# Kernel tuning notes

Measured on AMD Instinct MI355X. Metric: run time of the kernel, lower is better.

Reference implementation:

```python
import jax, jax.numpy as jnp
import numpy as np

BN_EPS = 1e-5

def _bn_relu(x, gamma, beta):
    # BatchNorm1d in training mode: batch stats over (B, N) per channel
    mean = jnp.mean(x, axis=(0, 1), keepdims=True)
    var = jnp.var(x, axis=(0, 1), keepdims=True)
    return jax.nn.relu((x - mean) * jax.lax.rsqrt(var + BN_EPS) * gamma + beta)

def setup_inputs() -> dict:
    key = jax.random.key(0)
    ks = jax.random.split(key, 8)
    B, N, S, C1, C2 = 8, 8192, 2048, 128, 256
    return {
        'xyz1': jax.random.normal(ks[0], (B, N, 3), jnp.float32),
        'xyz2': jax.random.normal(ks[1], (B, S, 3), jnp.float32),
        'points1': jax.random.normal(ks[2], (B, N, C1), jnp.float32),
        'points2': jax.random.normal(ks[3], (B, S, C2), jnp.float32),
        'w0': jax.random.normal(ks[4], (256, C1 + C2), jnp.float32) * 0.02,
        'b0': jnp.zeros((256,), jnp.float32),
        'g0': jnp.ones((256,), jnp.float32),
        'be0': jnp.zeros((256,), jnp.float32),
        'w1': jax.random.normal(ks[5], (128, 256), jnp.float32) * 0.02,
        'b1': jnp.zeros((128,), jnp.float32),
        'g1': jnp.ones((128,), jnp.float32),
        'be1': jnp.zeros((128,), jnp.float32),
    }

def reference(xyz1, xyz2, points1, points2, w0, b0, g0, be0, w1, b1, g1, be1):
    # squared pairwise distances [B, N, S]
    sq = (jnp.sum(xyz1 * xyz1, -1)[:, :, None]
          - 2.0 * jnp.einsum('bnc,bmc->bnm', xyz1, xyz2)
          + jnp.sum(xyz2 * xyz2, -1)[:, None, :])
    neg_d, idx = jax.lax.top_k(-sq, 3)          # smallest 3 distances
    dist = -neg_d                               # [B, N, 3]
    recip = 1.0 / (dist + 1e-8)
    weight = recip / jnp.sum(recip, -1, keepdims=True)
    gathered = jax.vmap(lambda p, i: p[i])(points2, idx)   # [B, N, 3, C2]
    interp = jnp.sum(gathered * weight[..., None], axis=2)  # [B, N, C2]
    x = jnp.concatenate([points1, interp], axis=-1)         # [B, N, C1+C2]
    x = _bn_relu(jnp.einsum('bnc,oc->bno', x, w0) + b0, g0, be0)
    x = _bn_relu(jnp.einsum('bnc,oc->bno', x, w1) + b1, g1, be1)
    return x
```

## Files before the change

kernel.cpp:

```cpp
#include <hip/hip_runtime.h>

#define B_  8
#define N_  8192
#define S_  2048
#define C1_ 128
#define C2_ 256
#define KA_ 384
#define H0_ 256
#define H1_ 128
#define R_  (B_ * N_)

typedef __bf16 bf16;
typedef __attribute__((ext_vector_type(4))) __bf16 bf16x4;
typedef __attribute__((ext_vector_type(8))) __bf16 bf16x8;
typedef __attribute__((ext_vector_type(4))) float f32x4;

__device__ __forceinline__ void gload_lds16(const void* g, void* l) {
    __builtin_amdgcn_global_load_lds(
        (const __attribute__((address_space(1))) void*)g,
        (__attribute__((address_space(3))) void*)l, 16, 0, 0);
}

__global__ void zero_kernel(float* __restrict__ p, int n) {
    int i = blockIdx.x * 256 + threadIdx.x;
    if (i < n) p[i] = 0.f;
}

__global__ __launch_bounds__(256) void cvt_kernel(const float* __restrict__ src,
                                                  bf16* __restrict__ dst, int n4) {
    int i = blockIdx.x * 256 + threadIdx.x;
    if (i < n4) {
        float4 v = *(const float4*)(src + (size_t)i * 4);
        bf16x4 o = { (bf16)v.x, (bf16)v.y, (bf16)v.z, (bf16)v.w };
        *(bf16x4*)(dst + (size_t)i * 4) = o;
    }
}

__global__ __launch_bounds__(256) void p1cvt_kernel(const float* __restrict__ p1,
                                                    bf16* __restrict__ Abf) {
    int e = blockIdx.x * 256 + threadIdx.x;
    int row = e >> 5, kc = e & 31;
    float4 v = *(const float4*)(p1 + (size_t)row * C1_ + kc * 4);
    bf16x4 o = { (bf16)v.x, (bf16)v.y, (bf16)v.z, (bf16)v.w };
    *(bf16x4*)(Abf + (size_t)row * KA_ + kc * 4) = o;
}

__global__ __launch_bounds__(256) void top3_kernel(
    const float* __restrict__ xyz1, const float* __restrict__ xyz2,
    int* __restrict__ out_idx, float* __restrict__ out_w)
{
    __shared__ float4 sc[S_];
    __shared__ float  md[64][4][3];
    __shared__ int    mi[64][4][3];

    int b = blockIdx.x >> 7;
    int ntile = blockIdx.x & 127;
    const float* src = xyz2 + (size_t)b * S_ * 3;
    for (int i = threadIdx.x; i < S_; i += 256) {
        float x = src[i * 3 + 0], y = src[i * 3 + 1], z = src[i * 3 + 2];
        float4 c; c.x = x; c.y = y; c.z = z; c.w = x * x + y * y + z * z;
        sc[i] = c;
    }
    __syncthreads();

    const int q  = threadIdx.x >> 2;
    const int sp = threadIdx.x & 3;
    const size_t row = (size_t)b * N_ + ntile * 64 + q;
    const float ax = -2.f * xyz1[row * 3 + 0];
    const float ay = -2.f * xyz1[row * 3 + 1];
    const float az = -2.f * xyz1[row * 3 + 2];

    float m0 = 1e30f, m1 = 1e30f, m2 = 1e30f;
    int   j0 = 0, j1 = 0, j2 = 0;

    #pragma unroll 4
    for (int i = 0; i < S_ / 4; ++i) {
        int s = i * 4 + sp;
        float4 c = sc[s];
        float m = fmaf(ax, c.x, fmaf(ay, c.y, fmaf(az, c.z, c.w)));
        if (m < m2) {
            if (m < m1) {
                m2 = m1; j2 = j1;
                if (m < m0) { m1 = m0; j1 = j0; m0 = m; j0 = s; }
                else        { m1 = m;  j1 = s; }
            } else { m2 = m; j2 = s; }
        }
    }
    md[q][sp][0] = m0; md[q][sp][1] = m1; md[q][sp][2] = m2;
    mi[q][sp][0] = j0; mi[q][sp][1] = j1; mi[q][sp][2] = j2;
    __syncthreads();

    if (threadIdx.x < 64) {
        int qq = threadIdx.x;
        float d0 = md[qq][0][0], d1 = md[qq][0][1], d2 = md[qq][0][2];
        int   i0 = mi[qq][0][0], i1 = mi[qq][0][1], i2 = mi[qq][0][2];
        #pragma unroll
        for (int p = 1; p < 4; ++p) {
            #pragma unroll
            for (int j = 0; j < 3; ++j) {
                float d = md[qq][p][j]; int s = mi[qq][p][j];
                bool lt2 = (d < d2) || (d == d2 && s < i2);
                if (lt2) {
                    bool lt1 = (d < d1) || (d == d1 && s < i1);
                    if (lt1) {
                        d2 = d1; i2 = i1;
                        bool lt0 = (d < d0) || (d == d0 && s < i0);
                        if (lt0) { d1 = d0; i1 = i0; d0 = d; i0 = s; }
                        else     { d1 = d;  i1 = s; }
                    } else { d2 = d; i2 = s; }
                }
            }
        }
        size_t orow = (size_t)b * N_ + ntile * 64 + qq;
        float px = xyz1[orow * 3 + 0], py = xyz1[orow * 3 + 1], pz = xyz1[orow * 3 + 2];
        float pp = px * px + py * py + pz * pz;
        float r0 = 1.f / (d0 + pp + 1e-8f);
        float r1 = 1.f / (d1 + pp + 1e-8f);
        float r2 = 1.f / (d2 + pp + 1e-8f);
        float inv = 1.f / (r0 + r1 + r2);
        out_idx[orow * 3 + 0] = i0; out_idx[orow * 3 + 1] = i1; out_idx[orow * 3 + 2] = i2;
        out_w[orow * 3 + 0] = r0 * inv; out_w[orow * 3 + 1] = r1 * inv; out_w[orow * 3 + 2] = r2 * inv;
    }
}

__global__ __launch_bounds__(256) void interp_kernel(
    const float* __restrict__ points2, const int* __restrict__ idx3,
    const float* __restrict__ w3, bf16* __restrict__ Abf)
{
    int t = threadIdx.x;
    size_t row = (size_t)blockIdx.x * 4 + (t >> 6);
    int lane = t & 63;
    int b = (int)(row >> 13);
    const float* p2 = points2 + (size_t)b * S_ * C2_;
    int ia = idx3[row * 3 + 0], ib = idx3[row * 3 + 1], ic = idx3[row * 3 + 2];
    float wa = w3[row * 3 + 0], wb = w3[row * 3 + 1], wc = w3[row * 3 + 2];
    float4 va = *(const float4*)(p2 + (size_t)ia * C2_ + lane * 4);
    float4 vb = *(const float4*)(p2 + (size_t)ib * C2_ + lane * 4);
    float4 vc = *(const float4*)(p2 + (size_t)ic * C2_ + lane * 4);
    bf16x4 o = { (bf16)(wa * va.x + wb * vb.x + wc * vc.x),
                 (bf16)(wa * va.y + wb * vb.y + wc * vc.y),
                 (bf16)(wa * va.z + wb * vb.z + wc * vc.z),
                 (bf16)(wa * va.w + wb * vb.w + wc * vc.w) };
    *(bf16x4*)(Abf + row * KA_ + C1_ + lane * 4) = o;
}

template<int K, int OT, bool OUTBF>
__global__ __launch_bounds__(256) void mfma_gemm_kernel(
    const bf16* __restrict__ A, const bf16* __restrict__ Wt, void* __restrict__ Cout)
{
    __shared__ bf16 As[128 * 32];
    __shared__ bf16 Bs[128 * 32];
    const int tid = threadIdx.x;
    const int lane = tid & 63, wave = tid >> 6;
    const int wr = wave >> 1, wc = wave & 1;
    const int r0 = blockIdx.x * 128, o0 = blockIdx.y * 128;

    f32x4 acc[4][4] = {};

    const int l15 = lane & 15, g = lane >> 4;
    const int slot = g ^ ((l15 >> 1) & 3);
    int a_off[4], b_off[4];
    #pragma unroll
    for (int m = 0; m < 4; ++m) a_off[m] = (wr * 64 + m * 16 + l15) * 32 + slot * 8;
    #pragma unroll
    for (int n = 0; n < 4; ++n) b_off[n] = (wc * 64 + n * 16 + l15) * 32 + slot * 8;

    const int c0 = tid, c1 = tid + 256;
    const int ar0 = c0 >> 2, ar1 = c1 >> 2;
    const int kb0 = ((c0 & 3) ^ ((ar0 >> 1) & 3)) * 8;
    const int kb1 = ((c1 & 3) ^ ((ar1 >> 1) & 3)) * 8;

    for (int k0 = 0; k0 < K; k0 += 32) {
        __syncthreads();
        gload_lds16(A  + (size_t)(r0 + ar0) * K + k0 + kb0, &As[c0 * 8]);
        gload_lds16(A  + (size_t)(r0 + ar1) * K + k0 + kb1, &As[c1 * 8]);
        gload_lds16(Wt + (size_t)(o0 + ar0) * K + k0 + kb0, &Bs[c0 * 8]);
        gload_lds16(Wt + (size_t)(o0 + ar1) * K + k0 + kb1, &Bs[c1 * 8]);
        __syncthreads();
        bf16x8 af[4], bfr[4];
        #pragma unroll
        for (int m = 0; m < 4; ++m) af[m]  = *(const bf16x8*)&As[a_off[m]];
        #pragma unroll
        for (int n = 0; n < 4; ++n) bfr[n] = *(const bf16x8*)&Bs[b_off[n]];
        #pragma unroll
        for (int m = 0; m < 4; ++m)
            #pragma unroll
            for (int n = 0; n < 4; ++n)
                acc[m][n] = __builtin_amdgcn_mfma_f32_16x16x32_bf16(af[m], bfr[n], acc[m][n], 0, 0, 0);
    }

    const int crow = r0 + wr * 64 + g * 4;
    const int ccol = o0 + wc * 64 + l15;
    #pragma unroll
    for (int m = 0; m < 4; ++m)
        #pragma unroll
        for (int n = 0; n < 4; ++n)
            #pragma unroll
            for (int j = 0; j < 4; ++j) {
                size_t off = (size_t)(crow + m * 16 + j) * OT + ccol + n * 16;
                if (OUTBF) ((bf16*)Cout)[off] = (bf16)acc[m][n][j];
                else       ((float*)Cout)[off] = acc[m][n][j];
            }
}

__global__ __launch_bounds__(256) void stats_bf16_kernel(const bf16* __restrict__ X,
                                                         float* __restrict__ sums,
                                                         float* __restrict__ sumsq)
{
    __shared__ float ls[256], lq[256];
    int tid = threadIdx.x;
    ls[tid] = 0.f; lq[tid] = 0.f;
    __syncthreads();
    int cg = tid & 31, rs = tid >> 5;
    size_t r0 = (size_t)blockIdx.x * 512 + rs;
    float s[8] = {}, q[8] = {};
    for (int i = 0; i < 64; ++i) {
        bf16x8 v = *(const bf16x8*)(X + (r0 + (size_t)i * 8) * 256 + cg * 8);
        #pragma unroll
        for (int j = 0; j < 8; ++j) { float f = (float)v[j]; s[j] += f; q[j] += f * f; }
    }
    #pragma unroll
    for (int j = 0; j < 8; ++j) {
        atomicAdd(&ls[cg * 8 + j], s[j]);
        atomicAdd(&lq[cg * 8 + j], q[j]);
    }
    __syncthreads();
    atomicAdd(&sums[tid], ls[tid]);
    atomicAdd(&sumsq[tid], lq[tid]);
}

__global__ __launch_bounds__(256) void stats_f32_kernel(const float* __restrict__ X,
                                                        float* __restrict__ sums,
                                                        float* __restrict__ sumsq)
{
    __shared__ float ls[128], lq[128];
    int tid = threadIdx.x;
    if (tid < 128) { ls[tid] = 0.f; lq[tid] = 0.f; }
    __syncthreads();
    int cg = tid & 31, rs = tid >> 5;
    size_t r0 = (size_t)blockIdx.x * 512 + rs;
    float s[4] = {}, q[4] = {};
    for (int i = 0; i < 64; ++i) {
        float4 v = *(const float4*)(X + (r0 + (size_t)i * 8) * 128 + cg * 4);
        s[0] += v.x; q[0] += v.x * v.x;
        s[1] += v.y; q[1] += v.y * v.y;
        s[2] += v.z; q[2] += v.z * v.z;
        s[3] += v.w; q[3] += v.w * v.w;
    }
    #pragma unroll
    for (int j = 0; j < 4; ++j) {
        atomicAdd(&ls[cg * 4 + j], s[j]);
        atomicAdd(&lq[cg * 4 + j], q[j]);
    }
    __syncthreads();
    if (tid < 128) {
        atomicAdd(&sums[tid], ls[tid]);
        atomicAdd(&sumsq[tid], lq[tid]);
    }
}

__global__ void finalize_kernel(const float* __restrict__ sums, const float* __restrict__ sumsq,
                                const float* __restrict__ g, const float* __restrict__ be,
                                float* __restrict__ scale, float* __restrict__ shift, float invR)
{
    int c = threadIdx.x;
    float mean = sums[c] * invR;
    float var = sumsq[c] * invR - mean * mean;
    float s = g[c] * rsqrtf(var + 1e-5f);
    scale[c] = s;
    shift[c] = be[c] - mean * s;
}

__global__ __launch_bounds__(256) void bnrelu_cvt_kernel(const bf16* __restrict__ hp,
                                                         const float* __restrict__ scale,
                                                         const float* __restrict__ shift,
                                                         bf16* __restrict__ hb)
{
    size_t i8 = (size_t)blockIdx.x * 256 + threadIdx.x;
    int c0 = (int)((i8 * 8) & (H0_ - 1));
    bf16x8 v = *(const bf16x8*)(hp + i8 * 8);
    bf16x8 o;
    #pragma unroll
    for (int j = 0; j < 8; ++j) {
        float f = (float)v[j];
        f = fmaxf(0.f, f * scale[c0 + j] + shift[c0 + j]);
        o[j] = (bf16)f;
    }
    *(bf16x8*)(hb + i8 * 8) = o;
}

__global__ __launch_bounds__(256) void bnrelu_kernel(float* __restrict__ X,
                                                     const float* __restrict__ scale,
                                                     const float* __restrict__ shift)
{
    size_t i = (size_t)blockIdx.x * 256 + threadIdx.x;
    float4 v = *(float4*)(X + i * 4);
    int c = (int)((i * 4) & (H1_ - 1));
    v.x = fmaxf(0.f, v.x * scale[c + 0] + shift[c + 0]);
    v.y = fmaxf(0.f, v.y * scale[c + 1] + shift[c + 1]);
    v.z = fmaxf(0.f, v.z * scale[c + 2] + shift[c + 2]);
    v.w = fmaxf(0.f, v.w * scale[c + 3] + shift[c + 3]);
    *(float4*)(X + i * 4) = v;
}

extern "C" void kernel_launch(void* const* d_in, const int* in_sizes, int n_in,
                              void* d_out, int out_size, void* d_ws, size_t ws_size,
                              hipStream_t stream)
{
    const float* xyz1    = (const float*)d_in[0];
    const float* xyz2    = (const float*)d_in[1];
    const float* points1 = (const float*)d_in[2];
    const float* points2 = (const float*)d_in[3];
    const float* w0  = (const float*)d_in[4];
    const float* g0  = (const float*)d_in[6];
    const float* be0 = (const float*)d_in[7];
    const float* w1  = (const float*)d_in[8];
    const float* g1  = (const float*)d_in[10];
    const float* be1 = (const float*)d_in[11];
    float* out = (float*)d_out;
    char* ws = (char*)d_ws;

    bf16* Abf     = (bf16*)(ws);
    bf16* hpre_bf = (bf16*)(ws + 50331648);
    bf16* hbf     = (bf16*)(ws + 83886080);
    bf16* Wbf0    = (bf16*)(ws + 117440512);
    bf16* Wbf1    = (bf16*)(ws + 117637120);
    int*  idx3    = (int*) (ws + 117702656);
    float* w3     = (float*)(ws + 118489088);
    float* stats  = (float*)(ws + 119275520);
    float* sums0 = stats,        *sumsq0 = stats + 256;
    float* sums1 = stats + 512,  *sumsq1 = stats + 640;
    float* scale0 = stats + 768,  *shift0 = stats + 1024;
    float* scale1 = stats + 1280, *shift1 = stats + 1408;

    zero_kernel<<<3, 256, 0, stream>>>(stats, 768);
    cvt_kernel<<<96, 256, 0, stream>>>(w0, Wbf0, H0_ * KA_ / 4);
    cvt_kernel<<<32, 256, 0, stream>>>(w1, Wbf1, H1_ * H0_ / 4);
    p1cvt_kernel<<<R_ * (C1_ / 4) / 256, 256, 0, stream>>>(points1, Abf);
    top3_kernel<<<B_ * (N_ / 64), 256, 0, stream>>>(xyz1, xyz2, idx3, w3);
    interp_kernel<<<R_ / 4, 256, 0, stream>>>(points2, idx3, w3, Abf);

    mfma_gemm_kernel<KA_, H0_, true><<<dim3(R_ / 128, 2), 256, 0, stream>>>(Abf, Wbf0, hpre_bf);
    stats_bf16_kernel<<<128, 256, 0, stream>>>(hpre_bf, sums0, sumsq0);
    finalize_kernel<<<1, 256, 0, stream>>>(sums0, sumsq0, g0, be0, scale0, shift0, 1.f / R_);
    bnrelu_cvt_kernel<<<R_ * H0_ / 8 / 256, 256, 0, stream>>>(hpre_bf, scale0, shift0, hbf);

    mfma_gemm_kernel<H0_, H1_, false><<<dim3(R_ / 128, 1), 256, 0, stream>>>(hbf, Wbf1, out);
    stats_f32_kernel<<<128, 256, 0, stream>>>(out, sums1, sumsq1);
    finalize_kernel<<<1, 128, 0, stream>>>(sums1, sumsq1, g1, be1, scale1, shift1, 1.f / R_);
    bnrelu_kernel<<<R_ * H1_ / 4 / 256, 256, 0, stream>>>(out, scale1, shift1);
}
```

Before: 187.8 us.

## Fuse BN statistics into GEMM epilogue and register-block top-3 search

```diff
diff --git a/kernel.cpp b/kernel.cpp
--- a/kernel.cpp
+++ b/kernel.cpp
@@ -21,6 +21,16 @@
         (__attribute__((address_space(3))) void*)l, 16, 0, 0);
 }
 
+__device__ __forceinline__ void ins3(float m, int s,
+                                     float& m0, float& m1, float& m2,
+                                     int& j0, int& j1, int& j2)
+{
+    bool b0 = m < m0, b1 = m < m1, b2 = m < m2;
+    m2 = b1 ? m1 : (b2 ? m : m2);  j2 = b1 ? j1 : (b2 ? s : j2);
+    m1 = b0 ? m0 : (b1 ? m : m1);  j1 = b0 ? j0 : (b1 ? s : j1);
+    m0 = b0 ? m  : m0;             j0 = b0 ? s  : j0;
+}
+
 __global__ void zero_kernel(float* __restrict__ p, int n) {
     int i = blockIdx.x * 256 + threadIdx.x;
     if (i < n) p[i] = 0.f;
@@ -50,8 +60,8 @@
     int* __restrict__ out_idx, float* __restrict__ out_w)
 {
     __shared__ float4 sc[S_];
-    __shared__ float  md[64][4][3];
-    __shared__ int    mi[64][4][3];
+    __shared__ float  md[64][8][3];
+    __shared__ int    mi[64][8][3];
 
     int b = blockIdx.x >> 7;
     int ntile = blockIdx.x & 127;
@@ -63,31 +73,34 @@
     }
     __syncthreads();
 
-    const int q  = threadIdx.x >> 2;
-    const int sp = threadIdx.x & 3;
-    const size_t row = (size_t)b * N_ + ntile * 64 + q;
-    const float ax = -2.f * xyz1[row * 3 + 0];
-    const float ay = -2.f * xyz1[row * 3 + 1];
-    const float az = -2.f * xyz1[row * 3 + 2];
-
-    float m0 = 1e30f, m1 = 1e30f, m2 = 1e30f;
-    int   j0 = 0, j1 = 0, j2 = 0;
+    const int qp = threadIdx.x >> 3;
+    const int sp = threadIdx.x & 7;
+    const size_t rowA = (size_t)b * N_ + ntile * 64 + qp * 2;
+    const float axA = -2.f * xyz1[rowA * 3 + 0];
+    const float ayA = -2.f * xyz1[rowA * 3 + 1];
+    const float azA = -2.f * xyz1[rowA * 3 + 2];
+    const float axB = -2.f * xyz1[rowA * 3 + 3];
+    const float ayB = -2.f * xyz1[rowA * 3 + 4];
+    const float azB = -2.f * xyz1[rowA * 3 + 5];
+
+    float a0 = 1e30f, a1 = 1e30f, a2 = 1e30f;
+    float e0 = 1e30f, e1 = 1e30f, e2 = 1e30f;
+    int   u0 = 0, u1 = 0, u2 = 0, v0 = 0, v1 = 0, v2 = 0;
 
     #pragma unroll 4
-    for (int i = 0; i < S_ / 4; ++i) {
-        int s = i * 4 + sp;
+    for (int i = 0; i < S_ / 8; ++i) {
+        int s = i * 8 + sp;
         float4 c = sc[s];
-        float m = fmaf(ax, c.x, fmaf(ay, c.y, fmaf(az, c.z, c.w)));
-        if (m < m2) {
-            if (m < m1) {
-                m2 = m1; j2 = j1;
-                if (m < m0) { m1 = m0; j1 = j0; m0 = m; j0 = s; }
-                else        { m1 = m;  j1 = s; }
-            } else { m2 = m; j2 = s; }
-        }
-    }
-    md[q][sp][0] = m0; md[q][sp][1] = m1; md[q][sp][2] = m2;
-    mi[q][sp][0] = j0; mi[q][sp][1] = j1; mi[q][sp][2] = j2;
+        float mA = fmaf(axA, c.x, fmaf(ayA, c.y, fmaf(azA, c.z, c.w)));
+        float mB = fmaf(axB, c.x, fmaf(ayB, c.y, fmaf(azB, c.z, c.w)));
+        ins3(mA, s, a0, a1, a2, u0, u1, u2);
+        ins3(mB, s, e0, e1, e2, v0, v1, v2);
+    }
+    int qa = qp * 2, qb = qa + 1;
+    md[qa][sp][0] = a0; md[qa][sp][1] = a1; md[qa][sp][2] = a2;
+    mi[qa][sp][0] = u0; mi[qa][sp][1] = u1; mi[qa][sp][2] = u2;
+    md[qb][sp][0] = e0; md[qb][sp][1] = e1; md[qb][sp][2] = e2;
+    mi[qb][sp][0] = v0; mi[qb][sp][1] = v1; mi[qb][sp][2] = v2;
     __syncthreads();
 
     if (threadIdx.x < 64) {
@@ -95,7 +108,7 @@
         float d0 = md[qq][0][0], d1 = md[qq][0][1], d2 = md[qq][0][2];
         int   i0 = mi[qq][0][0], i1 = mi[qq][0][1], i2 = mi[qq][0][2];
         #pragma unroll
-        for (int p = 1; p < 4; ++p) {
+        for (int p = 1; p < 8; ++p) {
             #pragma unroll
             for (int j = 0; j < 3; ++j) {
                 float d = md[qq][p][j]; int s = mi[qq][p][j];
@@ -146,10 +159,12 @@
 
 template<int K, int OT, bool OUTBF>
 __global__ __launch_bounds__(256) void mfma_gemm_kernel(
-    const bf16* __restrict__ A, const bf16* __restrict__ Wt, void* __restrict__ Cout)
+    const bf16* __restrict__ A, const bf16* __restrict__ Wt, void* __restrict__ Cout,
+    float* __restrict__ sums, float* __restrict__ sumsq)
 {
     __shared__ bf16 As[128 * 32];
     __shared__ bf16 Bs[128 * 32];
+    __shared__ float csum[128], csumsq[128];
     const int tid = threadIdx.x;
     const int lane = tid & 63, wave = tid >> 6;
     const int wr = wave >> 1, wc = wave & 1;
@@ -169,6 +184,8 @@
     const int ar0 = c0 >> 2, ar1 = c1 >> 2;
     const int kb0 = ((c0 & 3) ^ ((ar0 >> 1) & 3)) * 8;
     const int kb1 = ((c1 & 3) ^ ((ar1 >> 1) & 3)) * 8;
+
+    if (tid < 128) { csum[tid] = 0.f; csumsq[tid] = 0.f; }
 
     for (int k0 = 0; k0 < K; k0 += 32) {
         __syncthreads();
@@ -201,61 +218,25 @@
                 if (OUTBF) ((bf16*)Cout)[off] = (bf16)acc[m][n][j];
                 else       ((float*)Cout)[off] = acc[m][n][j];
             }
-}
-
-__global__ __launch_bounds__(256) void stats_bf16_kernel(const bf16* __restrict__ X,
-                                                         float* __restrict__ sums,
-                                                         float* __restrict__ sumsq)
-{
-    __shared__ float ls[256], lq[256];
-    int tid = threadIdx.x;
-    ls[tid] = 0.f; lq[tid] = 0.f;
-    __syncthreads();
-    int cg = tid & 31, rs = tid >> 5;
-    size_t r0 = (size_t)blockIdx.x * 512 + rs;
-    float s[8] = {}, q[8] = {};
-    for (int i = 0; i < 64; ++i) {
-        bf16x8 v = *(const bf16x8*)(X + (r0 + (size_t)i * 8) * 256 + cg * 8);
-        #pragma unroll
-        for (int j = 0; j < 8; ++j) { float f = (float)v[j]; s[j] += f; q[j] += f * f; }
-    }
-    #pragma unroll
-    for (int j = 0; j < 8; ++j) {
-        atomicAdd(&ls[cg * 8 + j], s[j]);
-        atomicAdd(&lq[cg * 8 + j], q[j]);
-    }
-    __syncthreads();
-    atomicAdd(&sums[tid], ls[tid]);
-    atomicAdd(&sumsq[tid], lq[tid]);
-}
-
-__global__ __launch_bounds__(256) void stats_f32_kernel(const float* __restrict__ X,
-                                                        float* __restrict__ sums,
-                                                        float* __restrict__ sumsq)
-{
-    __shared__ float ls[128], lq[128];
-    int tid = threadIdx.x;
-    if (tid < 128) { ls[tid] = 0.f; lq[tid] = 0.f; }
-    __syncthreads();
-    int cg = tid & 31, rs = tid >> 5;
-    size_t r0 = (size_t)blockIdx.x * 512 + rs;
-    float s[4] = {}, q[4] = {};
-    for (int i = 0; i < 64; ++i) {
-        float4 v = *(const float4*)(X + (r0 + (size_t)i * 8) * 128 + cg * 4);
-        s[0] += v.x; q[0] += v.x * v.x;
-        s[1] += v.y; q[1] += v.y * v.y;
-        s[2] += v.z; q[2] += v.z * v.z;
-        s[3] += v.w; q[3] += v.w * v.w;
-    }
-    #pragma unroll
-    for (int j = 0; j < 4; ++j) {
-        atomicAdd(&ls[cg * 4 + j], s[j]);
-        atomicAdd(&lq[cg * 4 + j], q[j]);
+
+    #pragma unroll
+    for (int n = 0; n < 4; ++n) {
+        float s = 0.f, q = 0.f;
+        #pragma unroll
+        for (int m = 0; m < 4; ++m)
+            #pragma unroll
+            for (int j = 0; j < 4; ++j) {
+                float v = acc[m][n][j];
+                s += v; q = fmaf(v, v, q);
+            }
+        int col = wc * 64 + n * 16 + l15;
+        atomicAdd(&csum[col], s);
+        atomicAdd(&csumsq[col], q);
     }
     __syncthreads();
     if (tid < 128) {
-        atomicAdd(&sums[tid], ls[tid]);
-        atomicAdd(&sumsq[tid], lq[tid]);
+        atomicAdd(&sums[o0 + tid], csum[tid]);
+        atomicAdd(&sumsq[o0 + tid], csumsq[tid]);
     }
 }
 
@@ -340,13 +321,13 @@
     top3_kernel<<<B_ * (N_ / 64), 256, 0, stream>>>(xyz1, xyz2, idx3, w3);
     interp_kernel<<<R_ / 4, 256, 0, stream>>>(points2, idx3, w3, Abf);
 
-    mfma_gemm_kernel<KA_, H0_, true><<<dim3(R_ / 128, 2), 256, 0, stream>>>(Abf, Wbf0, hpre_bf);
-    stats_bf16_kernel<<<128, 256, 0, stream>>>(hpre_bf, sums0, sumsq0);
+    mfma_gemm_kernel<KA_, H0_, true><<<dim3(R_ / 128, 2), 256, 0, stream>>>(
+        Abf, Wbf0, hpre_bf, sums0, sumsq0);
     finalize_kernel<<<1, 256, 0, stream>>>(sums0, sumsq0, g0, be0, scale0, shift0, 1.f / R_);
     bnrelu_cvt_kernel<<<R_ * H0_ / 8 / 256, 256, 0, stream>>>(hpre_bf, scale0, shift0, hbf);
 
-    mfma_gemm_kernel<H0_, H1_, false><<<dim3(R_ / 128, 1), 256, 0, stream>>>(hbf, Wbf1, out);
-    stats_f32_kernel<<<128, 256, 0, stream>>>(out, sums1, sumsq1);
+    mfma_gemm_kernel<H0_, H1_, false><<<dim3(R_ / 128, 1), 256, 0, stream>>>(
+        hbf, Wbf1, out, sums1, sumsq1);
     finalize_kernel<<<1, 128, 0, stream>>>(sums1, sumsq1, g1, be1, scale1, shift1, 1.f / R_);
     bnrelu_kernel<<<R_ * H1_ / 4 / 256, 256, 0, stream>>>(out, scale1, shift1);
 }
```

New measurement: 207.0 us. +10.2%, slower.

## Fuse BN stats into GEMM epilogues, BN-ReLU into GEMM2 prologue, p1 convert into interp

Applied to the files above, without the earlier changes.

```diff
diff --git a/kernel.cpp b/kernel.cpp
--- a/kernel.cpp
+++ b/kernel.cpp
@@ -11,6 +11,7 @@
 #define R_  (B_ * N_)
 
 typedef __bf16 bf16;
+typedef __attribute__((ext_vector_type(2))) __bf16 bf16x2;
 typedef __attribute__((ext_vector_type(4))) __bf16 bf16x4;
 typedef __attribute__((ext_vector_type(8))) __bf16 bf16x8;
 typedef __attribute__((ext_vector_type(4))) float f32x4;
@@ -34,15 +35,6 @@
         bf16x4 o = { (bf16)v.x, (bf16)v.y, (bf16)v.z, (bf16)v.w };
         *(bf16x4*)(dst + (size_t)i * 4) = o;
     }
-}
-
-__global__ __launch_bounds__(256) void p1cvt_kernel(const float* __restrict__ p1,
-                                                    bf16* __restrict__ Abf) {
-    int e = blockIdx.x * 256 + threadIdx.x;
-    int row = e >> 5, kc = e & 31;
-    float4 v = *(const float4*)(p1 + (size_t)row * C1_ + kc * 4);
-    bf16x4 o = { (bf16)v.x, (bf16)v.y, (bf16)v.z, (bf16)v.w };
-    *(bf16x4*)(Abf + (size_t)row * KA_ + kc * 4) = o;
 }
 
 __global__ __launch_bounds__(256) void top3_kernel(
@@ -124,8 +116,9 @@
 }
 
 __global__ __launch_bounds__(256) void interp_kernel(
-    const float* __restrict__ points2, const int* __restrict__ idx3,
-    const float* __restrict__ w3, bf16* __restrict__ Abf)
+    const float* __restrict__ points1, const float* __restrict__ points2,
+    const int* __restrict__ idx3, const float* __restrict__ w3,
+    bf16* __restrict__ Abf)
 {
     int t = threadIdx.x;
     size_t row = (size_t)blockIdx.x * 4 + (t >> 6);
@@ -142,14 +135,20 @@
                  (bf16)(wa * va.z + wb * vb.z + wc * vc.z),
                  (bf16)(wa * va.w + wb * vb.w + wc * vc.w) };
     *(bf16x4*)(Abf + row * KA_ + C1_ + lane * 4) = o;
+
+    float2 p = *(const float2*)(points1 + row * C1_ + lane * 2);
+    bf16x2 po = { (bf16)p.x, (bf16)p.y };
+    *(bf16x2*)(Abf + row * KA_ + lane * 2) = po;
 }
 
 template<int K, int OT, bool OUTBF>
 __global__ __launch_bounds__(256) void mfma_gemm_kernel(
-    const bf16* __restrict__ A, const bf16* __restrict__ Wt, void* __restrict__ Cout)
+    const bf16* __restrict__ A, const bf16* __restrict__ Wt, void* __restrict__ Cout,
+    float* __restrict__ sums, float* __restrict__ sumsq)
 {
     __shared__ bf16 As[128 * 32];
     __shared__ bf16 Bs[128 * 32];
+    __shared__ float csum[128], csumsq[128];
     const int tid = threadIdx.x;
     const int lane = tid & 63, wave = tid >> 6;
     const int wr = wave >> 1, wc = wave & 1;
@@ -169,6 +168,8 @@
     const int ar0 = c0 >> 2, ar1 = c1 >> 2;
     const int kb0 = ((c0 & 3) ^ ((ar0 >> 1) & 3)) * 8;
     const int kb1 = ((c1 & 3) ^ ((ar1 >> 1) & 3)) * 8;
+
+    if (tid < 128) { csum[tid] = 0.f; csumsq[tid] = 0.f; }
 
     for (int k0 = 0; k0 < K; k0 += 32) {
         __syncthreads();
@@ -201,61 +202,124 @@
                 if (OUTBF) ((bf16*)Cout)[off] = (bf16)acc[m][n][j];
                 else       ((float*)Cout)[off] = acc[m][n][j];
             }
-}
-
-__global__ __launch_bounds__(256) void stats_bf16_kernel(const bf16* __restrict__ X,
-                                                         float* __restrict__ sums,
-                                                         float* __restrict__ sumsq)
-{
-    __shared__ float ls[256], lq[256];
-    int tid = threadIdx.x;
-    ls[tid] = 0.f; lq[tid] = 0.f;
-    __syncthreads();
-    int cg = tid & 31, rs = tid >> 5;
-    size_t r0 = (size_t)blockIdx.x * 512 + rs;
-    float s[8] = {}, q[8] = {};
-    for (int i = 0; i < 64; ++i) {
-        bf16x8 v = *(const bf16x8*)(X + (r0 + (size_t)i * 8) * 256 + cg * 8);
-        #pragma unroll
-        for (int j = 0; j < 8; ++j) { float f = (float)v[j]; s[j] += f; q[j] += f * f; }
-    }
-    #pragma unroll
-    for (int j = 0; j < 8; ++j) {
-        atomicAdd(&ls[cg * 8 + j], s[j]);
-        atomicAdd(&lq[cg * 8 + j], q[j]);
-    }
-    __syncthreads();
-    atomicAdd(&sums[tid], ls[tid]);
-    atomicAdd(&sumsq[tid], lq[tid]);
-}
-
-__global__ __launch_bounds__(256) void stats_f32_kernel(const float* __restrict__ X,
-                                                        float* __restrict__ sums,
-                                                        float* __restrict__ sumsq)
-{
-    __shared__ float ls[128], lq[128];
-    int tid = threadIdx.x;
-    if (tid < 128) { ls[tid] = 0.f; lq[tid] = 0.f; }
-    __syncthreads();
-    int cg = tid & 31, rs = tid >> 5;
-    size_t r0 = (size_t)blockIdx.x * 512 + rs;
-    float s[4] = {}, q[4] = {};
-    for (int i = 0; i < 64; ++i) {
-        float4 v = *(const float4*)(X + (r0 + (size_t)i * 8) * 128 + cg * 4);
-        s[0] += v.x; q[0] += v.x * v.x;
-        s[1] += v.y; q[1] += v.y * v.y;
-        s[2] += v.z; q[2] += v.z * v.z;
-        s[3] += v.w; q[3] += v.w * v.w;
-    }
-    #pragma unroll
-    for (int j = 0; j < 4; ++j) {
-        atomicAdd(&ls[cg * 4 + j], s[j]);
-        atomicAdd(&lq[cg * 4 + j], q[j]);
+
+    #pragma unroll
+    for (int n = 0; n < 4; ++n) {
+        float s = 0.f, q = 0.f;
+        #pragma unroll
+        for (int m = 0; m < 4; ++m)
+            #pragma unroll
+            for (int j = 0; j < 4; ++j) {
+                float v = acc[m][n][j];
+                s += v; q = fmaf(v, v, q);
+            }
+        int col = wc * 64 + n * 16 + l15;
+        atomicAdd(&csum[col], s);
+        atomicAdd(&csumsq[col], q);
     }
     __syncthreads();
     if (tid < 128) {
-        atomicAdd(&sums[tid], ls[tid]);
-        atomicAdd(&sumsq[tid], lq[tid]);
+        atomicAdd(&sums[o0 + tid], csum[tid]);
+        atomicAdd(&sumsq[o0 + tid], csumsq[tid]);
+    }
+}
+
+__global__ __launch_bounds__(256) void mfma_gemm2_kernel(
+    const bf16* __restrict__ Ahp, const bf16* __restrict__ Wt,
+    const float* __restrict__ scale, const float* __restrict__ shift,
+    float* __restrict__ Cout, float* __restrict__ sums, float* __restrict__ sumsq)
+{
+    constexpr int K = H0_, OT = H1_;
+    __shared__ bf16 As[128 * 32];
+    __shared__ bf16 Bs[128 * 32];
+    __shared__ float csum[128], csumsq[128];
+    const int tid = threadIdx.x;
+    const int lane = tid & 63, wave = tid >> 6;
+    const int wr = wave >> 1, wc = wave & 1;
+    const int r0 = blockIdx.x * 128, o0 = blockIdx.y * 128;
+
+    f32x4 acc[4][4] = {};
+
+    const int l15 = lane & 15, g = lane >> 4;
+    const int slot = g ^ ((l15 >> 1) & 3);
+    int a_off[4], b_off[4];
+    #pragma unroll
+    for (int m = 0; m < 4; ++m) a_off[m] = (wr * 64 + m * 16 + l15) * 32 + slot * 8;
+    #pragma unroll
+    for (int n = 0; n < 4; ++n) b_off[n] = (wc * 64 + n * 16 + l15) * 32 + slot * 8;
+
+    const int c0 = tid, c1 = tid + 256;
+    const int ar0 = c0 >> 2, ar1 = c1 >> 2;
+    const int kb0 = ((c0 & 3) ^ ((ar0 >> 1) & 3)) * 8;
+    const int kb1 = ((c1 & 3) ^ ((ar1 >> 1) & 3)) * 8;
+
+    if (tid < 128) { csum[tid] = 0.f; csumsq[tid] = 0.f; }
+
+    for (int k0 = 0; k0 < K; k0 += 32) {
+        bf16x8 va0 = *(const bf16x8*)(Ahp + (size_t)(r0 + ar0) * K + k0 + kb0);
+        bf16x8 va1 = *(const bf16x8*)(Ahp + (size_t)(r0 + ar1) * K + k0 + kb1);
+        float s0a[8], h0a[8], s1a[8], h1a[8];
+        *(float4*)&s0a[0] = *(const float4*)(scale + k0 + kb0);
+        *(float4*)&s0a[4] = *(const float4*)(scale + k0 + kb0 + 4);
+        *(float4*)&h0a[0] = *(const float4*)(shift + k0 + kb0);
+        *(float4*)&h0a[4] = *(const float4*)(shift + k0 + kb0 + 4);
+        *(float4*)&s1a[0] = *(const float4*)(scale + k0 + kb1);
+        *(float4*)&s1a[4] = *(const float4*)(scale + k0 + kb1 + 4);
+        *(float4*)&h1a[0] = *(const float4*)(shift + k0 + kb1);
+        *(float4*)&h1a[4] = *(const float4*)(shift + k0 + kb1 + 4);
+        bf16x8 ra0, ra1;
+        #pragma unroll
+        for (int j = 0; j < 8; ++j) {
+            float f0 = fmaxf(0.f, fmaf((float)va0[j], s0a[j], h0a[j]));
+            float f1 = fmaxf(0.f, fmaf((float)va1[j], s1a[j], h1a[j]));
+            ra0[j] = (bf16)f0; ra1[j] = (bf16)f1;
+        }
+        __syncthreads();
+        gload_lds16(Wt + (size_t)(o0 + ar0) * K + k0 + kb0, &Bs[c0 * 8]);
+        gload_lds16(Wt + (size_t)(o0 + ar1) * K + k0 + kb1, &Bs[c1 * 8]);
+        *(bf16x8*)&As[c0 * 8] = ra0;
+        *(bf16x8*)&As[c1 * 8] = ra1;
+        __syncthreads();
+        bf16x8 af[4], bfr[4];
+        #pragma unroll
+        for (int m = 0; m < 4; ++m) af[m]  = *(const bf16x8*)&As[a_off[m]];
+        #pragma unroll
+        for (int n = 0; n < 4; ++n) bfr[n] = *(const bf16x8*)&Bs[b_off[n]];
+        #pragma unroll
+        for (int m = 0; m < 4; ++m)
+            #pragma unroll
+            for (int n = 0; n < 4; ++n)
+                acc[m][n] = __builtin_amdgcn_mfma_f32_16x16x32_bf16(af[m], bfr[n], acc[m][n], 0, 0, 0);
+    }
+
+    const int crow = r0 + wr * 64 + g * 4;
+    const int ccol = o0 + wc * 64 + l15;
+    #pragma unroll
+    for (int m = 0; m < 4; ++m)
+        #pragma unroll
+        for (int n = 0; n < 4; ++n)
+            #pragma unroll
+            for (int j = 0; j < 4; ++j)
+                ((float*)Cout)[(size_t)(crow + m * 16 + j) * OT + ccol + n * 16] = acc[m][n][j];
+
+    #pragma unroll
+    for (int n = 0; n < 4; ++n) {
+        float s = 0.f, q = 0.f;
+        #pragma unroll
+        for (int m = 0; m < 4; ++m)
+            #pragma unroll
+            for (int j = 0; j < 4; ++j) {
+                float v = acc[m][n][j];
+                s += v; q = fmaf(v, v, q);
+            }
+        int col = wc * 64 + n * 16 + l15;
+        atomicAdd(&csum[col], s);
+        atomicAdd(&csumsq[col], q);
+    }
+    __syncthreads();
+    if (tid < 128) {
+        atomicAdd(&sums[o0 + tid], csum[tid]);
+        atomicAdd(&sumsq[o0 + tid], csumsq[tid]);
     }
 }
 
@@ -269,24 +333,6 @@
     float s = g[c] * rsqrtf(var + 1e-5f);
     scale[c] = s;
     shift[c] = be[c] - mean * s;
-}
-
-__global__ __launch_bounds__(256) void bnrelu_cvt_kernel(const bf16* __restrict__ hp,
-                                                         const float* __restrict__ scale,
-                                                         const float* __restrict__ shift,
-                                                         bf16* __restrict__ hb)
-{
-    size_t i8 = (size_t)blockIdx.x * 256 + threadIdx.x;
-    int c0 = (int)((i8 * 8) & (H0_ - 1));
-    bf16x8 v = *(const bf16x8*)(hp + i8 * 8);
-    bf16x8 o;
-    #pragma unroll
-    for (int j = 0; j < 8; ++j) {
-        float f = (float)v[j];
-        f = fmaxf(0.f, f * scale[c0 + j] + shift[c0 + j]);
-        o[j] = (bf16)f;
-    }
-    *(bf16x8*)(hb + i8 * 8) = o;
 }
 
 __global__ __launch_bounds__(256) void bnrelu_kernel(float* __restrict__ X,
@@ -322,7 +368,6 @@
 
     bf16* Abf     = (bf16*)(ws);
     bf16* hpre_bf = (bf16*)(ws + 50331648);
-    bf16* hbf     = (bf16*)(ws + 83886080);
     bf16* Wbf0    = (bf16*)(ws + 117440512);
     bf16* Wbf1    = (bf16*)(ws + 117637120);
     int*  idx3    = (int*) (ws + 117702656);
@@ -336,17 +381,15 @@
     zero_kernel<<<3, 256, 0, stream>>>(stats, 768);
     cvt_kernel<<<96, 256, 0, stream>>>(w0, Wbf0, H0_ * KA_ / 4);
     cvt_kernel<<<32, 256, 0, stream>>>(w1, Wbf1, H1_ * H0_ / 4);
-    p1cvt_kernel<<<R_ * (C1_ / 4) / 256, 256, 0, stream>>>(points1, Abf);
     top3_kernel<<<B_ * (N_ / 64), 256, 0, stream>>>(xyz1, xyz2, idx3, w3);
-    interp_kernel<<<R_ / 4, 256, 0, stream>>>(points2, idx3, w3, Abf);
-
-    mfma_gemm_kernel<KA_, H0_, true><<<dim3(R_ / 128, 2), 256, 0, stream>>>(Abf, Wbf0, hpre_bf);
-    stats_bf16_kernel<<<128, 256, 0, stream>>>(hpre_bf, sums0, sumsq0);
+    interp_kernel<<<R_ / 4, 256, 0, stream>>>(points1, points2, idx3, w3, Abf);
+
+    mfma_gemm_kernel<KA_, H0_, true><<<dim3(R_ / 128, 2), 256, 0, stream>>>(
+        Abf, Wbf0, hpre_bf, sums0, sumsq0);
     finalize_kernel<<<1, 256, 0, stream>>>(sums0, sumsq0, g0, be0, scale0, shift0, 1.f / R_);
-    bnrelu_cvt_kernel<<<R_ * H0_ / 8 / 256, 256, 0, stream>>>(hpre_bf, scale0, shift0, hbf);
-
-    mfma_gemm_kernel<H0_, H1_, false><<<dim3(R_ / 128, 1), 256, 0, stream>>>(hbf, Wbf1, out);
-    stats_f32_kernel<<<128, 256, 0, stream>>>(out, sums1, sumsq1);
+
+    mfma_gemm2_kernel<<<dim3(R_ / 128, 1), 256, 0, stream>>>(
+        hpre_bf, Wbf1, scale0, shift0, out, sums1, sumsq1);
     finalize_kernel<<<1, 128, 0, stream>>>(sums1, sumsq1, g1, be1, scale1, shift1, 1.f / R_);
     bnrelu_kernel<<<R_ * H1_ / 4 / 256, 256, 0, stream>>>(out, scale1, shift1);
 }
```

Result: faster. 183.9 us (-2.1%).
